# Kernel tuning notes

Measured on AMD Instinct MI355X. Metric: run time of the kernel, lower is better.

Reference implementation:

```python
import jax, jax.numpy as jnp
import numpy as np

D_MODEL = 768
D_FF = 3072
N_HEADS = 12
D_QUART = D_MODEL // 4  # 192
EPS = 1e-5


def layer_norm(x, g, b):
    mu = jnp.mean(x, axis=-1, keepdims=True)
    var = jnp.mean((x - mu) ** 2, axis=-1, keepdims=True)
    return (x - mu) * jax.lax.rsqrt(var + EPS) * g + b


def setup_inputs() -> dict:
    key = jax.random.key(0)
    ks = jax.random.split(key, 24)
    d, dff, dq = D_MODEL, D_FF, D_QUART
    s = lambda k, shape, fan: jax.random.normal(k, shape, jnp.float32) * (1.0 / np.sqrt(fan))
    return {
        "x": jax.random.normal(ks[0], (8, 1024, d), jnp.float32),
        # distance_proj: Linear(1, d//4) -> weight [dq], bias [dq]
        "dp_w": s(ks[1], (dq,), 1), "dp_b": jnp.zeros((dq,), jnp.float32),
        # spatial_encoding: Linear(d,d) GELU Linear(d,d)
        "se_w1": s(ks[2], (d, d), d), "se_b1": jnp.zeros((d,), jnp.float32),
        "se_w2": s(ks[3], (d, d), d), "se_b2": jnp.zeros((d,), jnp.float32),
        # attention projections (stored [in, out])
        "wq": s(ks[4], (d, d), d), "bq": jnp.zeros((d,), jnp.float32),
        "wk": s(ks[5], (d, d), d), "bk": jnp.zeros((d,), jnp.float32),
        "wv": s(ks[6], (d, d), d), "bv": jnp.zeros((d,), jnp.float32),
        "wo": s(ks[7], (d, d), d), "bo": jnp.zeros((d,), jnp.float32),
        # geometric_net FFN
        "gw1": s(ks[8], (d, dff), d), "gb1": jnp.zeros((dff,), jnp.float32),
        "gw2": s(ks[9], (dff, d), dff), "gb2": jnp.zeros((d,), jnp.float32),
        # layer norms
        "n1_g": jnp.ones((d,), jnp.float32), "n1_b": jnp.zeros((d,), jnp.float32),
        "n2_g": jnp.ones((d,), jnp.float32), "n2_b": jnp.zeros((d,), jnp.float32),
    }


def _forward(x, dp_w, dp_b, se_w1, se_b1, se_w2, se_b2,
             wq, bq, wk, bk, wv, bv, wo, bo,
             gw1, gb1, gw2, gb2, n1_g, n1_b, n2_g, n2_b):
    B, N, d = x.shape
    # --- compute_spatial_features ---
    # ||x_i - x_j|| via Gram trick (avoids [B,N,N,d] intermediate)
    sq = jnp.sum(x * x, axis=-1)                      # [B,N]
    gram = jnp.einsum('bnd,bmd->bnm', x, x)           # [B,N,N]
    d2 = jnp.maximum(sq[:, :, None] + sq[:, None, :] - 2.0 * gram, 0.0)
    dist = jnp.sqrt(d2)                               # [B,N,N]
    # Linear(1, d/4) then mean over j commutes: project the mean distance
    mean_d = jnp.mean(dist, axis=2)                   # [B,N]
    spat = mean_d[..., None] * dp_w + dp_b            # [B,N,d/4]
    spat = jnp.pad(spat, ((0, 0), (0, 0), (0, d - D_QUART)))  # [B,N,d]
    # spatial_encoding MLP (exact GELU, matching torch nn.GELU default)
    h = jax.nn.gelu(spat @ se_w1 + se_b1, approximate=False)
    x = x + (h @ se_w2 + se_b2)
    # --- attention block ---
    res = x
    xn = layer_norm(x, n1_g, n1_b)
    H, dh = N_HEADS, d // N_HEADS
    q = (xn @ wq + bq).reshape(B, N, H, dh)
    k = (xn @ wk + bk).reshape(B, N, H, dh)
    v = (xn @ wv + bv).reshape(B, N, H, dh)
    scores = jnp.einsum('bqhd,bkhd->bhqk', q, k) / np.sqrt(dh)
    attn = jax.nn.softmax(scores, axis=-1)
    o = jnp.einsum('bhqk,bkhd->bqhd', attn, v).reshape(B, N, d)
    x = res + (o @ wo + bo)
    # --- FFN block ---
    res = x
    xn = layer_norm(x, n2_g, n2_b)
    h = jax.nn.gelu(xn @ gw1 + gb1, approximate=False)
    x = res + (h @ gw2 + gb2)
    return x


def reference(x, dp_w, dp_b, se_w1, se_b1, se_w2, se_b2,
              wq, bq, wk, bk, wv, bv, wo, bo,
              gw1, gb1, gw2, gb2, n1_g, n1_b, n2_g, n2_b):
    return _forward(x, dp_w, dp_b, se_w1, se_b1, se_w2, se_b2,
                    wq, bq, wk, bk, wv, bv, wo, bo,
                    gw1, gb1, gw2, gb2, n1_g, n1_b, n2_g, n2_b)
```

## Files before the change

kernel.cpp:

```cpp
#include <hip/hip_runtime.h>
#include <hip/hip_bf16.h>

typedef unsigned short ushort;
typedef __attribute__((ext_vector_type(8))) __bf16 bf16x8;
typedef __attribute__((ext_vector_type(4))) float f32x4;
typedef __attribute__((ext_vector_type(8))) ushort ushort8;

__device__ inline ushort f2bf(float f) {
    union { float f; unsigned u; } a{f};
    unsigned r = a.u + 0x7FFFu + ((a.u >> 16) & 1u);
    return (ushort)(r >> 16);
}
__device__ inline float gelu_f(float x) {
    return 0.5f * x * (1.f + erff(x * 0.70710678118654752f));
}

__global__ void transpose_to_bf16(const float* __restrict__ Wm, ushort* __restrict__ Wt, int K, int N) {
    __shared__ float tile[32][33];
    int k0 = blockIdx.x * 32, n0 = blockIdx.y * 32;
    int tx = threadIdx.x, ty = threadIdx.y;
    #pragma unroll
    for (int r = ty; r < 32; r += 8) tile[r][tx] = Wm[(size_t)(k0 + r) * N + n0 + tx];
    __syncthreads();
    #pragma unroll
    for (int r = ty; r < 32; r += 8) Wt[(size_t)(n0 + r) * K + k0 + tx] = f2bf(tile[tx][r]);
}

__global__ void rowstat(const float* __restrict__ x, ushort* __restrict__ xb, float* __restrict__ sq) {
    int row = blockIdx.x;
    const float* xr = x + (size_t)row * 768;
    ushort* xbr = xb + (size_t)row * 768;
    int t = threadIdx.x;
    float s = 0.f;
    #pragma unroll
    for (int i = 0; i < 3; ++i) {
        float vv = xr[t + i * 256];
        xbr[t + i * 256] = f2bf(vv);
        s += vv * vv;
    }
    #pragma unroll
    for (int off = 1; off < 64; off <<= 1) s += __shfl_xor(s, off);
    __shared__ float wsum[4];
    if ((t & 63) == 0) wsum[t >> 6] = s;
    __syncthreads();
    if (t == 0) sq[row] = wsum[0] + wsum[1] + wsum[2] + wsum[3];
}

__global__ void precomp_ac(const float* __restrict__ dp_w, const float* __restrict__ dp_b,
                           const float* __restrict__ se_w1, const float* __restrict__ se_b1,
                           float* __restrict__ Avec, float* __restrict__ Cvec) {
    int o = blockIdx.x * 256 + threadIdx.x;
    float a = 0.f, c = 0.f;
    for (int i = 0; i < 192; ++i) {
        float w = se_w1[(size_t)i * 768 + o];
        a += dp_w[i] * w;
        c += dp_b[i] * w;
    }
    Avec[o] = a;
    Cvec[o] = c + se_b1[o];
}

__global__ void hgen(const float* __restrict__ mean_acc, const float* __restrict__ Avec,
                     const float* __restrict__ Cvec, ushort* __restrict__ h) {
    int row = blockIdx.x;
    float md = mean_acc[row] * (1.f / 1024.f);
    int t = threadIdx.x;
    #pragma unroll
    for (int i = 0; i < 3; ++i) {
        int o = t + i * 256;
        h[(size_t)row * 768 + o] = f2bf(gelu_f(md * Avec[o] + Cvec[o]));
    }
}

__global__ void lnorm(const float* __restrict__ xin, const float* __restrict__ g,
                      const float* __restrict__ b, ushort* __restrict__ xn) {
    int row = blockIdx.x;
    const float* xr = xin + (size_t)row * 768;
    int t = threadIdx.x;
    float v[3];
    float s = 0.f, s2 = 0.f;
    #pragma unroll
    for (int i = 0; i < 3; ++i) {
        v[i] = xr[t + i * 256];
        s += v[i];
        s2 += v[i] * v[i];
    }
    #pragma unroll
    for (int off = 1; off < 64; off <<= 1) { s += __shfl_xor(s, off); s2 += __shfl_xor(s2, off); }
    __shared__ float a0[4], a1[4];
    if ((t & 63) == 0) { a0[t >> 6] = s; a1[t >> 6] = s2; }
    __syncthreads();
    s = a0[0] + a0[1] + a0[2] + a0[3];
    s2 = a1[0] + a1[1] + a1[2] + a1[3];
    float mu = s * (1.f / 768.f);
    float var = s2 * (1.f / 768.f) - mu * mu;
    float rs = rsqrtf(var + 1e-5f);
    #pragma unroll
    for (int i = 0; i < 3; ++i) {
        int o = t + i * 256;
        xn[(size_t)row * 768 + o] = f2bf((v[i] - mu) * rs * g[o] + b[o]);
    }
}

#define BM 128
#define BK 32

enum { EPI_BF16 = 0, EPI_GELU = 1, EPI_RES = 2, EPI_GRAM = 3, EPI_QKV = 4 };

template <int EPI, int BNT>
__launch_bounds__(256, BNT == 64 ? 4 : 2)
__global__ void gemm_bt(const ushort* __restrict__ A, const ushort* __restrict__ Bt,
                        int M, int N, int K,
                        const float* __restrict__ bias,
                        const float* res, float* outf,
                        ushort* __restrict__ outh,
                        const float* __restrict__ sq, float* __restrict__ mean_acc) {
    __shared__ __align__(16) ushort As[2][BM * BK];
    __shared__ __align__(16) ushort Bs[2][BNT * BK];

    unsigned gx = gridDim.x, gy = gridDim.y;
    unsigned flat = blockIdx.x + gx * (blockIdx.y + gy * blockIdx.z);
    unsigned total = gx * gy * gridDim.z;
    unsigned chunk = total >> 3;
    flat = (flat & 7) * chunk + (flat >> 3);
    unsigned bx = flat % gx;
    unsigned rem = flat / gx;
    unsigned by = rem % gy;
    unsigned bz = rem / gy;

    int m0 = bx * BM;
    int n0 = by * BNT;
    if (EPI == EPI_GRAM) {
        A += (size_t)bz * 1024 * 768;
        Bt = A;
        sq += bz * 1024;
        mean_acc += bz * 1024;
    }
    int t = threadIdx.x, w = t >> 6, l = t & 63;
    int lg = l >> 4, li = l & 15;
    constexpr int MI = (BNT == 128) ? 4 : 2;
    int wm = (BNT == 128) ? (w >> 1) * 64 : w * 32;
    int wn = (BNT == 128) ? (w & 1) * 64 : 0;

    int srow = l >> 2, scol = (l & 3) * 8;
    const ushort* agp0 = A + (size_t)(m0 + (2 * w) * 16 + srow) * K + scol;
    const ushort* agp1 = A + (size_t)(m0 + (2 * w + 1) * 16 + srow) * K + scol;
    const ushort* bgp0;
    const ushort* bgp1 = nullptr;
    ushort* la0 = &As[0][(2 * w) * 16 * BK];
    ushort* lb0;
    if (BNT == 128) {
        bgp0 = Bt + (size_t)(n0 + (2 * w) * 16 + srow) * K + scol;
        bgp1 = Bt + (size_t)(n0 + (2 * w + 1) * 16 + srow) * K + scol;
        lb0 = &Bs[0][(2 * w) * 16 * BK];
    } else {
        bgp0 = Bt + (size_t)(n0 + w * 16 + srow) * K + scol;
        lb0 = &Bs[0][w * 16 * BK];
    }

    f32x4 acc[MI][4] = {};

    auto stage = [&](int buf, int kt) {
        size_t ko = (size_t)kt * BK;
        ushort* la = la0 + buf * (BM * BK);
        ushort* lb = lb0 + buf * (BNT * BK);
        __builtin_amdgcn_global_load_lds((const __attribute__((address_space(1))) void*)(agp0 + ko),
                                         (__attribute__((address_space(3))) void*)la, 16, 0, 0);
        __builtin_amdgcn_global_load_lds((const __attribute__((address_space(1))) void*)(agp1 + ko),
                                         (__attribute__((address_space(3))) void*)(la + 16 * BK), 16, 0, 0);
        __builtin_amdgcn_global_load_lds((const __attribute__((address_space(1))) void*)(bgp0 + ko),
                                         (__attribute__((address_space(3))) void*)lb, 16, 0, 0);
        if (BNT == 128)
            __builtin_amdgcn_global_load_lds((const __attribute__((address_space(1))) void*)(bgp1 + ko),
                                             (__attribute__((address_space(3))) void*)(lb + 16 * BK), 16, 0, 0);
    };

    int nk = K / BK;
    stage(0, 0);
    __syncthreads();
    int buf = 0;
    for (int kt = 0; kt < nk; ++kt) {
        if (kt + 1 < nk) stage(buf ^ 1, kt + 1);
        bf16x8 af[MI], bfr[4];
        #pragma unroll
        for (int i = 0; i < MI; ++i)
            af[i] = *reinterpret_cast<const bf16x8*>(&As[buf][(wm + i * 16 + li) * BK + lg * 8]);
        #pragma unroll
        for (int i = 0; i < 4; ++i)
            bfr[i] = *reinterpret_cast<const bf16x8*>(&Bs[buf][(wn + i * 16 + li) * BK + lg * 8]);
        #pragma unroll
        for (int mi = 0; mi < MI; ++mi)
            #pragma unroll
            for (int ni = 0; ni < 4; ++ni)
                acc[mi][ni] = __builtin_amdgcn_mfma_f32_16x16x32_bf16(af[mi], bfr[ni], acc[mi][ni], 0, 0, 0);
        __syncthreads();
        buf ^= 1;
    }

    #pragma unroll
    for (int mi = 0; mi < MI; ++mi) {
        #pragma unroll
        for (int r = 0; r < 4; ++r) {
            int row = m0 + wm + mi * 16 + lg * 4 + r;
            if (EPI == EPI_GRAM) {
                float si = sq[row];
                float s = 0.f;
                #pragma unroll
                for (int ni = 0; ni < 4; ++ni) {
                    int col = n0 + wn + ni * 16 + li;
                    float d2 = si + sq[col] - 2.f * acc[mi][ni][r];
                    s += sqrtf(fmaxf(d2, 0.f));
                }
                s += __shfl_xor(s, 1); s += __shfl_xor(s, 2);
                s += __shfl_xor(s, 4); s += __shfl_xor(s, 8);
                if (li == 0) atomicAdd(&mean_acc[row], s);
            } else {
                #pragma unroll
                for (int ni = 0; ni < 4; ++ni) {
                    int col = n0 + wn + ni * 16 + li;
                    float v = acc[mi][ni][r] + bias[col];
                    if (EPI == EPI_BF16) outh[(size_t)row * N + col] = f2bf(v);
                    if (EPI == EPI_GELU) outh[(size_t)row * N + col] = f2bf(gelu_f(v));
                    if (EPI == EPI_RES) outf[(size_t)row * N + col] = res[(size_t)row * N + col] + v;
                    if (EPI == EPI_QKV) {
                        int which = col / 768;
                        int c2 = col - which * 768;
                        outh[(size_t)which * (8192 * 768) + (size_t)row * 768 + c2] = f2bf(v);
                    }
                }
            }
        }
    }
}

template <int EPI>
__launch_bounds__(512, 2)
__global__ void gemm8(const ushort* __restrict__ A, const ushort* __restrict__ Bt,
                      int M, int N, int K,
                      const float* __restrict__ bias,
                      const float* res, float* outf, ushort* __restrict__ outh) {
    __shared__ __align__(16) ushort As[3][2][128 * 64];
    __shared__ __align__(16) ushort Bs[3][2][64 * 64];

    unsigned gx = gridDim.x;
    unsigned orig = blockIdx.x + gx * blockIdx.y;
    unsigned xcd = orig & 7;
    unsigned q = orig >> 3;
    unsigned mpg = gx >> 3;
    unsigned mloc = q % mpg;
    unsigned n = q / mpg;
    int m0 = (xcd * mpg + mloc) * 256;
    int n0 = n * 128;

    int t = threadIdx.x, w = t >> 6, l = t & 63;
    int lg = l >> 4, li = l & 15;
    int wr = w >> 1, wc = w & 1;
    int ha = wr >> 1;
    int ra = (wr & 1) * 64;

    f32x4 acc[4][4] = {};

    auto stage = [&](int buf, int kt) {
        int k0 = kt * 64;
        #pragma unroll
        for (int h = 0; h < 2; ++h) {
            #pragma unroll
            for (int jj = 0; jj < 2; ++jj) {
                int d = (2 * w + jj) * 1024 + l * 16;
                int dp = d ^ (((d >> 7) & 7) << 4);
                const ushort* src = A + (size_t)(m0 + h * 128 + (dp >> 7)) * K + k0 + ((dp & 127) >> 1);
                __builtin_amdgcn_global_load_lds(
                    (const __attribute__((address_space(1))) void*)src,
                    (__attribute__((address_space(3))) void*)&As[buf][h][(2 * w + jj) * 512], 16, 0, 0);
            }
            {
                int d = w * 1024 + l * 16;
                int dp = d ^ (((d >> 7) & 7) << 4);
                const ushort* src = Bt + (size_t)(n0 + h * 64 + (dp >> 7)) * K + k0 + ((dp & 127) >> 1);
                __builtin_amdgcn_global_load_lds(
                    (const __attribute__((address_space(1))) void*)src,
                    (__attribute__((address_space(3))) void*)&Bs[buf][h][w * 512], 16, 0, 0);
            }
        }
    };

    int nk = K / 64;
    stage(0, 0);
    stage(1, 1);
    stage(2, 2);
    for (int kt = 0; kt < nk; ++kt) {
        int buf = kt % 3;
        if (kt + 2 < nk)      asm volatile("s_waitcnt vmcnt(12)" ::: "memory");
        else if (kt + 1 < nk) asm volatile("s_waitcnt vmcnt(6)" ::: "memory");
        else                  asm volatile("s_waitcnt vmcnt(0)" ::: "memory");
        asm volatile("s_barrier" ::: "memory");
        __builtin_amdgcn_sched_barrier(0);
        #pragma unroll
        for (int kk = 0; kk < 2; ++kk) {
            bf16x8 af[4], bf[4];
            #pragma unroll
            for (int mi = 0; mi < 4; ++mi) {
                int e = (ra + mi * 16 + li) * 128 + kk * 64 + lg * 16;
                int ep = e ^ (((e >> 7) & 7) << 4);
                af[mi] = *reinterpret_cast<const bf16x8*>(&As[buf][ha][ep >> 1]);
            }
            #pragma unroll
            for (int ni = 0; ni < 4; ++ni) {
                int e = (ni * 16 + li) * 128 + kk * 64 + lg * 16;
                int ep = e ^ (((e >> 7) & 7) << 4);
                bf[ni] = *reinterpret_cast<const bf16x8*>(&Bs[buf][wc][ep >> 1]);
            }
            __builtin_amdgcn_s_setprio(1);
            #pragma unroll
            for (int mi = 0; mi < 4; ++mi)
                #pragma unroll
                for (int ni = 0; ni < 4; ++ni)
                    acc[mi][ni] = __builtin_amdgcn_mfma_f32_16x16x32_bf16(af[mi], bf[ni], acc[mi][ni], 0, 0, 0);
            __builtin_amdgcn_s_setprio(0);
        }
        asm volatile("s_barrier" ::: "memory");
        __builtin_amdgcn_sched_barrier(0);
        if (kt + 3 < nk) stage(buf, kt + 3);
    }

    #pragma unroll
    for (int mi = 0; mi < 4; ++mi) {
        #pragma unroll
        for (int r = 0; r < 4; ++r) {
            int row = m0 + wr * 64 + mi * 16 + lg * 4 + r;
            #pragma unroll
            for (int ni = 0; ni < 4; ++ni) {
                int col = n0 + wc * 64 + ni * 16 + li;
                float v = acc[mi][ni][r] + bias[col];
                if (EPI == EPI_GELU) outh[(size_t)row * N + col] = f2bf(gelu_f(v));
                if (EPI == EPI_RES)  outf[(size_t)row * N + col] = res[(size_t)row * N + col] + v;
                if (EPI == EPI_QKV) {
                    int which = col / 768;
                    int c2 = col - which * 768;
                    outh[(size_t)which * (8192 * 768) + (size_t)row * 768 + c2] = f2bf(v);
                }
            }
        }
    }
}

__launch_bounds__(256, 3)
__global__ void flash_attn(const ushort* __restrict__ q, const ushort* __restrict__ k,
                           const ushort* __restrict__ v, ushort* __restrict__ o) {
    int flat = blockIdx.x + 8 * (blockIdx.y + 12 * blockIdx.z);
    flat = (flat & 7) * 96 + (flat >> 3);
    int qt = flat & 7;
    int rem = flat >> 3;
    int h = rem % 12;
    int b = rem / 12;

    int t = threadIdx.x, w = t >> 6, l = t & 63;
    int lg = l >> 4, li = l & 15;

    __shared__ __align__(16) ushort Vt[2][64][72];
    __shared__ __align__(16) ushort P[4][32][72];

    const size_t hoff = (size_t)h * 64;
    const size_t bbase = (size_t)b * 1024 * 768;

    bf16x8 qf[2][2];
    #pragma unroll
    for (int f = 0; f < 2; ++f) {
        int qrow = qt * 128 + w * 32 + f * 16 + li;
        const ushort* qp = &q[bbase + (size_t)qrow * 768 + hoff];
        qf[f][0] = *reinterpret_cast<const bf16x8*>(qp + lg * 8);
        qf[f][1] = *reinterpret_cast<const bf16x8*>(qp + 32 + lg * 8);
    }

    float m_[2][4], ell[2][4];
    f32x4 oacc[2][4];
    #pragma unroll
    for (int f = 0; f < 2; ++f)
        #pragma unroll
        for (int r = 0; r < 4; ++r) { m_[f][r] = -1e30f; ell[f][r] = 0.f; }
    #pragma unroll
    for (int f = 0; f < 2; ++f)
        #pragma unroll
        for (int n = 0; n < 4; ++n) oacc[f][n] = f32x4{0.f, 0.f, 0.f, 0.f};

    int vrow = t & 63;
    int vc = t >> 6;
    const ushort* vbase = &v[bbase + hoff];

    ushort8 vv0 = *reinterpret_cast<const ushort8*>(&vbase[(size_t)vrow * 768 + vc * 8]);
    ushort8 vv1 = *reinterpret_cast<const ushort8*>(&vbase[(size_t)vrow * 768 + (vc + 4) * 8]);

    for (int jt = 0; jt < 16; ++jt) {
        int j0 = jt * 64, buf = jt & 1;
        #pragma unroll
        for (int i = 0; i < 8; ++i) Vt[buf][vc * 8 + i][vrow] = vv0[i];
        #pragma unroll
        for (int i = 0; i < 8; ++i) Vt[buf][(vc + 4) * 8 + i][vrow] = vv1[i];
        if (jt < 15) {
            vv0 = *reinterpret_cast<const ushort8*>(&vbase[(size_t)(j0 + 64 + vrow) * 768 + vc * 8]);
            vv1 = *reinterpret_cast<const ushort8*>(&vbase[(size_t)(j0 + 64 + vrow) * 768 + (vc + 4) * 8]);
        }
        bf16x8 kf0[4], kf1[4];
        #pragma unroll
        for (int jj = 0; jj < 4; ++jj) {
            const ushort* kp = &k[bbase + (size_t)(j0 + jj * 16 + li) * 768 + hoff];
            kf0[jj] = *reinterpret_cast<const bf16x8*>(kp + lg * 8);
            kf1[jj] = *reinterpret_cast<const bf16x8*>(kp + 32 + lg * 8);
        }
        f32x4 s[2][4];
        #pragma unroll
        for (int jj = 0; jj < 4; ++jj)
            #pragma unroll
            for (int f = 0; f < 2; ++f) {
                f32x4 a = {0.f, 0.f, 0.f, 0.f};
                a = __builtin_amdgcn_mfma_f32_16x16x32_bf16(qf[f][0], kf0[jj], a, 0, 0, 0);
                a = __builtin_amdgcn_mfma_f32_16x16x32_bf16(qf[f][1], kf1[jj], a, 0, 0, 0);
                s[f][jj] = a * 0.125f;
            }
        #pragma unroll
        for (int f = 0; f < 2; ++f) {
            float mt[4];
            #pragma unroll
            for (int r = 0; r < 4; ++r)
                mt[r] = fmaxf(fmaxf(s[f][0][r], s[f][1][r]), fmaxf(s[f][2][r], s[f][3][r]));
            #pragma unroll
            for (int r = 0; r < 4; ++r) {
                mt[r] = fmaxf(mt[r], __shfl_xor(mt[r], 1));
                mt[r] = fmaxf(mt[r], __shfl_xor(mt[r], 2));
                mt[r] = fmaxf(mt[r], __shfl_xor(mt[r], 4));
                mt[r] = fmaxf(mt[r], __shfl_xor(mt[r], 8));
            }
            float al[4], ps[4];
            #pragma unroll
            for (int r = 0; r < 4; ++r) {
                float mn = fmaxf(m_[f][r], mt[r]);
                al[r] = __expf(m_[f][r] - mn);
                m_[f][r] = mn;
                float p0 = __expf(s[f][0][r] - mn);
                float p1 = __expf(s[f][1][r] - mn);
                float p2 = __expf(s[f][2][r] - mn);
                float p3 = __expf(s[f][3][r] - mn);
                s[f][0][r] = p0; s[f][1][r] = p1; s[f][2][r] = p2; s[f][3][r] = p3;
                ps[r] = (p0 + p1) + (p2 + p3);
            }
            #pragma unroll
            for (int r = 0; r < 4; ++r) {
                ps[r] += __shfl_xor(ps[r], 1); ps[r] += __shfl_xor(ps[r], 2);
                ps[r] += __shfl_xor(ps[r], 4); ps[r] += __shfl_xor(ps[r], 8);
                ell[f][r] = ell[f][r] * al[r] + ps[r];
            }
            #pragma unroll
            for (int n = 0; n < 4; ++n)
                #pragma unroll
                for (int r = 0; r < 4; ++r) oacc[f][n][r] *= al[r];
            #pragma unroll
            for (int jj = 0; jj < 4; ++jj)
                #pragma unroll
                for (int r = 0; r < 4; ++r)
                    P[w][f * 16 + lg * 4 + r][jj * 16 + li] = f2bf(s[f][jj][r]);
        }
        __syncthreads();
        bf16x8 pf[2][2];
        #pragma unroll
        for (int f = 0; f < 2; ++f) {
            pf[f][0] = *reinterpret_cast<const bf16x8*>(&P[w][f * 16 + li][lg * 8]);
            pf[f][1] = *reinterpret_cast<const bf16x8*>(&P[w][f * 16 + li][32 + lg * 8]);
        }
        #pragma unroll
        for (int n = 0; n < 4; ++n) {
            bf16x8 vf0 = *reinterpret_cast<const bf16x8*>(&Vt[buf][n * 16 + li][lg * 8]);
            bf16x8 vf1 = *reinterpret_cast<const bf16x8*>(&Vt[buf][n * 16 + li][32 + lg * 8]);
            #pragma unroll
            for (int f = 0; f < 2; ++f) {
                oacc[f][n] = __builtin_amdgcn_mfma_f32_16x16x32_bf16(pf[f][0], vf0, oacc[f][n], 0, 0, 0);
                oacc[f][n] = __builtin_amdgcn_mfma_f32_16x16x32_bf16(pf[f][1], vf1, oacc[f][n], 0, 0, 0);
            }
        }
    }
    #pragma unroll
    for (int f = 0; f < 2; ++f)
        #pragma unroll
        for (int n = 0; n < 4; ++n)
            #pragma unroll
            for (int r = 0; r < 4; ++r) {
                int row = qt * 128 + w * 32 + f * 16 + lg * 4 + r;
                o[bbase + (size_t)row * 768 + hoff + n * 16 + li] = f2bf(oacc[f][n][r] / ell[f][r]);
            }
}

extern "C" void kernel_launch(void* const* d_in, const int* in_sizes, int n_in,
                              void* d_out, int out_size, void* d_ws, size_t ws_size,
                              hipStream_t stream) {
    const float* x = (const float*)d_in[0];
    const float* dp_w = (const float*)d_in[1];
    const float* dp_b = (const float*)d_in[2];
    const float* se_w1 = (const float*)d_in[3];
    const float* se_b1 = (const float*)d_in[4];
    const float* se_w2 = (const float*)d_in[5];
    const float* se_b2 = (const float*)d_in[6];
    const float* wq = (const float*)d_in[7];  const float* bq = (const float*)d_in[8];
    const float* wk = (const float*)d_in[9];  const float* bk = (const float*)d_in[10];
    const float* wv = (const float*)d_in[11]; const float* bv = (const float*)d_in[12];
    const float* wo = (const float*)d_in[13]; const float* bo = (const float*)d_in[14];
    const float* gw1 = (const float*)d_in[15]; const float* gb1 = (const float*)d_in[16];
    const float* gw2 = (const float*)d_in[17]; const float* gb2 = (const float*)d_in[18];
    const float* n1g = (const float*)d_in[19]; const float* n1b = (const float*)d_in[20];
    const float* n2g = (const float*)d_in[21]; const float* n2b = (const float*)d_in[22];
    float* out = (float*)d_out;

    constexpr size_t SZ_ACT = (size_t)8192 * 768 * 2;
    char* W = (char*)d_ws;
    ushort* xb = (ushort*)(W);
    ushort* q_ = (ushort*)(W + SZ_ACT);
    ushort* k_ = (ushort*)(W + 2 * SZ_ACT);
    ushort* v_ = (ushort*)(W + 3 * SZ_ACT);
    ushort* o_ = (ushort*)(W + 4 * SZ_ACT);
    ushort* hsp = q_;
    ushort* hff = q_;
    ushort* wqt = (ushort*)(W + 5 * SZ_ACT);
    ushort* wkt = wqt + (size_t)768 * 768;
    ushort* wvt = wkt + (size_t)768 * 768;
    ushort* wot = wvt + (size_t)768 * 768;
    ushort* sw2t = wot + (size_t)768 * 768;
    ushort* g1t = sw2t + (size_t)768 * 768;
    ushort* g2t = g1t + (size_t)768 * 3072;
    float* sqv = (float*)(g2t + (size_t)3072 * 768);
    float* meanv = sqv + 8192;
    float* Avec = meanv + 8192;
    float* Cvec = Avec + 768;
    float* bqkv = Cvec + 768;

    dim3 tb(32, 8);
    transpose_to_bf16<<<dim3(24, 24), tb, 0, stream>>>(se_w2, sw2t, 768, 768);
    transpose_to_bf16<<<dim3(24, 24), tb, 0, stream>>>(wq, wqt, 768, 768);
    transpose_to_bf16<<<dim3(24, 24), tb, 0, stream>>>(wk, wkt, 768, 768);
    transpose_to_bf16<<<dim3(24, 24), tb, 0, stream>>>(wv, wvt, 768, 768);
    transpose_to_bf16<<<dim3(24, 24), tb, 0, stream>>>(wo, wot, 768, 768);
    transpose_to_bf16<<<dim3(24, 96), tb, 0, stream>>>(gw1, g1t, 768, 3072);
    transpose_to_bf16<<<dim3(96, 24), tb, 0, stream>>>(gw2, g2t, 3072, 768);
    hipMemcpyAsync(bqkv, bq, 768 * sizeof(float), hipMemcpyDeviceToDevice, stream);
    hipMemcpyAsync(bqkv + 768, bk, 768 * sizeof(float), hipMemcpyDeviceToDevice, stream);
    hipMemcpyAsync(bqkv + 1536, bv, 768 * sizeof(float), hipMemcpyDeviceToDevice, stream);

    rowstat<<<8192, 256, 0, stream>>>(x, xb, sqv);
    precomp_ac<<<3, 256, 0, stream>>>(dp_w, dp_b, se_w1, se_b1, Avec, Cvec);
    hipMemsetAsync(meanv, 0, 8192 * sizeof(float), stream);

    gemm_bt<EPI_GRAM, 128><<<dim3(8, 8, 8), 256, 0, stream>>>(xb, xb, 1024, 1024, 768,
                                                              nullptr, nullptr, nullptr, nullptr, sqv, meanv);
    hgen<<<8192, 256, 0, stream>>>(meanv, Avec, Cvec, hsp);
    gemm8<EPI_RES><<<dim3(32, 6), 512, 0, stream>>>(hsp, sw2t, 8192, 768, 768,
                                                    se_b2, x, out, nullptr);
    lnorm<<<8192, 256, 0, stream>>>(out, n1g, n1b, xb);
    gemm8<EPI_QKV><<<dim3(32, 18), 512, 0, stream>>>(xb, wqt, 8192, 2304, 768,
                                                     bqkv, nullptr, nullptr, q_);
    flash_attn<<<dim3(8, 12, 8), 256, 0, stream>>>(q_, k_, v_, o_);
    gemm8<EPI_RES><<<dim3(32, 6), 512, 0, stream>>>(o_, wot, 8192, 768, 768,
                                                    bo, out, out, nullptr);
    lnorm<<<8192, 256, 0, stream>>>(out, n2g, n2b, xb);
    gemm8<EPI_GELU><<<dim3(32, 24), 512, 0, stream>>>(xb, g1t, 8192, 3072, 768,
                                                      gb1, nullptr, nullptr, hff);
    gemm8<EPI_RES><<<dim3(32, 6), 512, 0, stream>>>(hff, g2t, 8192, 768, 3072,
                                                    gb2, out, out, nullptr);
}
```

Measured before the change: 475.9 us.

## Split flash attention over two KV halves and merge partials

The flash attention kernel now splits each query tile's key/value range into two halves, doubling the grid from 768 to 1536 blocks for better CU occupancy, and raises launch bounds to 4 blocks per CU. Each half writes unnormalized bf16 partial outputs plus per-row max and sum, and a new merge kernel combines them with log-sum-exp rescaling. This adds an extra kernel launch, partial-output traffic through the xb buffer, and some rounding error from storing unnormalized partials in bf16.

```diff
diff --git a/kernel.cpp b/kernel.cpp
--- a/kernel.cpp
+++ b/kernel.cpp
@@ -10,6 +10,10 @@
     union { float f; unsigned u; } a{f};
     unsigned r = a.u + 0x7FFFu + ((a.u >> 16) & 1u);
     return (ushort)(r >> 16);
+}
+__device__ inline float bf2f(ushort u) {
+    union { unsigned u; float f; } a{(unsigned)u << 16};
+    return a.f;
 }
 __device__ inline float gelu_f(float x) {
     return 0.5f * x * (1.f + erff(x * 0.70710678118654752f));
@@ -344,13 +348,16 @@
     }
 }
 
-__launch_bounds__(256, 3)
+__launch_bounds__(256, 4)
 __global__ void flash_attn(const ushort* __restrict__ q, const ushort* __restrict__ k,
-                           const ushort* __restrict__ v, ushort* __restrict__ o) {
-    int flat = blockIdx.x + 8 * (blockIdx.y + 12 * blockIdx.z);
-    flat = (flat & 7) * 96 + (flat >> 3);
+                           const ushort* __restrict__ v,
+                           ushort* __restrict__ po0, ushort* __restrict__ po1,
+                           float* __restrict__ pm, float* __restrict__ pe) {
+    int flat = blockIdx.x + 16 * (blockIdx.y + 12 * blockIdx.z);
+    flat = (flat & 7) * 192 + (flat >> 3);
     int qt = flat & 7;
-    int rem = flat >> 3;
+    int split = (flat >> 3) & 1;
+    int rem = flat >> 4;
     int h = rem % 12;
     int b = rem / 12;
 
@@ -387,16 +394,17 @@
     int vc = t >> 6;
     const ushort* vbase = &v[bbase + hoff];
 
-    ushort8 vv0 = *reinterpret_cast<const ushort8*>(&vbase[(size_t)vrow * 768 + vc * 8]);
-    ushort8 vv1 = *reinterpret_cast<const ushort8*>(&vbase[(size_t)vrow * 768 + (vc + 4) * 8]);
-
-    for (int jt = 0; jt < 16; ++jt) {
+    const int jts = split * 8;
+    ushort8 vv0 = *reinterpret_cast<const ushort8*>(&vbase[(size_t)(jts * 64 + vrow) * 768 + vc * 8]);
+    ushort8 vv1 = *reinterpret_cast<const ushort8*>(&vbase[(size_t)(jts * 64 + vrow) * 768 + (vc + 4) * 8]);
+
+    for (int jt = jts; jt < jts + 8; ++jt) {
         int j0 = jt * 64, buf = jt & 1;
         #pragma unroll
         for (int i = 0; i < 8; ++i) Vt[buf][vc * 8 + i][vrow] = vv0[i];
         #pragma unroll
         for (int i = 0; i < 8; ++i) Vt[buf][(vc + 4) * 8 + i][vrow] = vv1[i];
-        if (jt < 15) {
+        if (jt < jts + 7) {
             vv0 = *reinterpret_cast<const ushort8*>(&vbase[(size_t)(j0 + 64 + vrow) * 768 + vc * 8]);
             vv1 = *reinterpret_cast<const ushort8*>(&vbase[(size_t)(j0 + 64 + vrow) * 768 + (vc + 4) * 8]);
         }
@@ -477,6 +485,7 @@
             }
         }
     }
+    ushort* po = split ? po1 : po0;
     #pragma unroll
     for (int f = 0; f < 2; ++f)
         #pragma unroll
@@ -484,8 +493,47 @@
             #pragma unroll
             for (int r = 0; r < 4; ++r) {
                 int row = qt * 128 + w * 32 + f * 16 + lg * 4 + r;
-                o[bbase + (size_t)row * 768 + hoff + n * 16 + li] = f2bf(oacc[f][n][r] / ell[f][r]);
-            }
+                po[bbase + (size_t)row * 768 + hoff + n * 16 + li] = f2bf(oacc[f][n][r]);
+            }
+    if (li == 0) {
+        #pragma unroll
+        for (int f = 0; f < 2; ++f)
+            #pragma unroll
+            for (int r = 0; r < 4; ++r) {
+                int rowl = qt * 128 + w * 32 + f * 16 + lg * 4 + r;
+                size_t si = (((size_t)split * 8 + b) * 12 + h) * 1024 + rowl;
+                pm[si] = m_[f][r];
+                pe[si] = ell[f][r];
+            }
+    }
+}
+
+__launch_bounds__(128)
+__global__ void merge_attn(const ushort* __restrict__ po0, const ushort* __restrict__ po1,
+                           const float* __restrict__ pm, const float* __restrict__ pe,
+                           ushort* __restrict__ o) {
+    int row = blockIdx.x;
+    int b = row >> 10, n = row & 1023;
+    int t = threadIdx.x;
+    if (t >= 96) return;
+    int c = t * 8;
+    int h = c >> 6;
+    size_t si0 = ((size_t)b * 12 + h) * 1024 + n;
+    size_t si1 = ((size_t)(8 + b) * 12 + h) * 1024 + n;
+    float m0 = pm[si0], m1 = pm[si1];
+    float e0 = pe[si0], e1 = pe[si1];
+    float m = fmaxf(m0, m1);
+    float a0 = __expf(m0 - m), a1 = __expf(m1 - m);
+    float inv = 1.f / (a0 * e0 + a1 * e1);
+    a0 *= inv; a1 *= inv;
+    size_t idx = (size_t)row * 768 + c;
+    ushort8 u0 = *reinterpret_cast<const ushort8*>(&po0[idx]);
+    ushort8 u1 = *reinterpret_cast<const ushort8*>(&po1[idx]);
+    ushort8 rr;
+    #pragma unroll
+    for (int i = 0; i < 8; ++i)
+        rr[i] = f2bf(a0 * bf2f(u0[i]) + a1 * bf2f(u1[i]));
+    *reinterpret_cast<ushort8*>(&o[idx]) = rr;
 }
 
 extern "C" void kernel_launch(void* const* d_in, const int* in_sizes, int n_in,
@@ -529,6 +577,8 @@
     float* Avec = meanv + 8192;
     float* Cvec = Avec + 768;
     float* bqkv = Cvec + 768;
+    float* pm = bqkv + 2304;
+    float* pe = pm + 2 * 8 * 12 * 1024;
 
     dim3 tb(32, 8);
     transpose_to_bf16<<<dim3(24, 24), tb, 0, stream>>>(se_w2, sw2t, 768, 768);
@@ -554,7 +604,8 @@
     lnorm<<<8192, 256, 0, stream>>>(out, n1g, n1b, xb);
     gemm8<EPI_QKV><<<dim3(32, 18), 512, 0, stream>>>(xb, wqt, 8192, 2304, 768,
                                                      bqkv, nullptr, nullptr, q_);
-    flash_attn<<<dim3(8, 12, 8), 256, 0, stream>>>(q_, k_, v_, o_);
+    flash_attn<<<dim3(16, 12, 8), 256, 0, stream>>>(q_, k_, v_, o_, xb, pm, pe);
+    merge_attn<<<8192, 128, 0, stream>>>(o_, xb, pm, pe, o_);
     gemm8<EPI_RES><<<dim3(32, 6), 512, 0, stream>>>(o_, wot, 8192, 768, 768,
                                                     bo, out, out, nullptr);
     lnorm<<<8192, 256, 0, stream>>>(out, n2g, n2b, xb);
```

After: 492.5 us. 1.04x slower.

## Use lazy max rescaling and MFMA row-sum in flash attention softmax

Applied to the files above, without the earlier changes.

Changes the online softmax in the attention kernel in two ways. The running max and output rescale are updated only when some row's new tile max exceeds the stored max by more than a threshold of 8, otherwise exponentials use the stale max. The per-row sum of probabilities is now computed by an extra MFMA against a ones vector instead of shuffle reductions. This removes shuffles and per-tile rescaling work, at the cost of extra MFMAs, a wave-wide branch, and a possible loss of precision because probabilities up to e^8 are stored in bf16.

```diff
diff --git a/kernel.cpp b/kernel.cpp
--- a/kernel.cpp
+++ b/kernel.cpp
@@ -372,16 +372,21 @@
         qf[f][1] = *reinterpret_cast<const bf16x8*>(qp + 32 + lg * 8);
     }
 
-    float m_[2][4], ell[2][4];
+    bf16x8 onesf;
+    #pragma unroll
+    for (int i = 0; i < 8; ++i) onesf[i] = (__bf16)1.0f;
+
+    float m_[2][4];
     f32x4 oacc[2][4];
-    #pragma unroll
-    for (int f = 0; f < 2; ++f)
-        #pragma unroll
-        for (int r = 0; r < 4; ++r) { m_[f][r] = -1e30f; ell[f][r] = 0.f; }
-    #pragma unroll
-    for (int f = 0; f < 2; ++f)
+    f32x4 oell[2];
+    #pragma unroll
+    for (int f = 0; f < 2; ++f) {
+        #pragma unroll
+        for (int r = 0; r < 4; ++r) m_[f][r] = -1e30f;
+        oell[f] = f32x4{0.f, 0.f, 0.f, 0.f};
         #pragma unroll
         for (int n = 0; n < 4; ++n) oacc[f][n] = f32x4{0.f, 0.f, 0.f, 0.f};
+    }
 
     int vrow = t & 63;
     int vc = t >> 6;
@@ -430,34 +435,24 @@
                 mt[r] = fmaxf(mt[r], __shfl_xor(mt[r], 4));
                 mt[r] = fmaxf(mt[r], __shfl_xor(mt[r], 8));
             }
-            float al[4], ps[4];
-            #pragma unroll
-            for (int r = 0; r < 4; ++r) {
-                float mn = fmaxf(m_[f][r], mt[r]);
-                al[r] = __expf(m_[f][r] - mn);
-                m_[f][r] = mn;
-                float p0 = __expf(s[f][0][r] - mn);
-                float p1 = __expf(s[f][1][r] - mn);
-                float p2 = __expf(s[f][2][r] - mn);
-                float p3 = __expf(s[f][3][r] - mn);
-                s[f][0][r] = p0; s[f][1][r] = p1; s[f][2][r] = p2; s[f][3][r] = p3;
-                ps[r] = (p0 + p1) + (p2 + p3);
-            }
-            #pragma unroll
-            for (int r = 0; r < 4; ++r) {
-                ps[r] += __shfl_xor(ps[r], 1); ps[r] += __shfl_xor(ps[r], 2);
-                ps[r] += __shfl_xor(ps[r], 4); ps[r] += __shfl_xor(ps[r], 8);
-                ell[f][r] = ell[f][r] * al[r] + ps[r];
-            }
-            #pragma unroll
-            for (int n = 0; n < 4; ++n)
+            bool need = (mt[0] > m_[f][0] + 8.f) | (mt[1] > m_[f][1] + 8.f) |
+                        (mt[2] > m_[f][2] + 8.f) | (mt[3] > m_[f][3] + 8.f);
+            if (__any(need)) {
                 #pragma unroll
-                for (int r = 0; r < 4; ++r) oacc[f][n][r] *= al[r];
+                for (int r = 0; r < 4; ++r) {
+                    float mn = fmaxf(m_[f][r], mt[r]);
+                    float al = __expf(m_[f][r] - mn);
+                    m_[f][r] = mn;
+                    #pragma unroll
+                    for (int n = 0; n < 4; ++n) oacc[f][n][r] *= al;
+                    oell[f][r] *= al;
+                }
+            }
             #pragma unroll
             for (int jj = 0; jj < 4; ++jj)
                 #pragma unroll
                 for (int r = 0; r < 4; ++r)
-                    P[w][f * 16 + lg * 4 + r][jj * 16 + li] = f2bf(s[f][jj][r]);
+                    P[w][f * 16 + lg * 4 + r][jj * 16 + li] = f2bf(__expf(s[f][jj][r] - m_[f][r]));
         }
         __syncthreads();
         bf16x8 pf[2][2];
@@ -467,6 +462,11 @@
             pf[f][1] = *reinterpret_cast<const bf16x8*>(&P[w][f * 16 + li][32 + lg * 8]);
         }
         #pragma unroll
+        for (int f = 0; f < 2; ++f) {
+            oell[f] = __builtin_amdgcn_mfma_f32_16x16x32_bf16(pf[f][0], onesf, oell[f], 0, 0, 0);
+            oell[f] = __builtin_amdgcn_mfma_f32_16x16x32_bf16(pf[f][1], onesf, oell[f], 0, 0, 0);
+        }
+        #pragma unroll
         for (int n = 0; n < 4; ++n) {
             bf16x8 vf0 = *reinterpret_cast<const bf16x8*>(&Vt[buf][n * 16 + li][lg * 8]);
             bf16x8 vf1 = *reinterpret_cast<const bf16x8*>(&Vt[buf][n * 16 + li][32 + lg * 8]);
@@ -484,7 +484,7 @@
             #pragma unroll
             for (int r = 0; r < 4; ++r) {
                 int row = qt * 128 + w * 32 + f * 16 + lg * 4 + r;
-                o[bbase + (size_t)row * 768 + hoff + n * 16 + li] = f2bf(oacc[f][n][r] / ell[f][r]);
+                o[bbase + (size_t)row * 768 + hoff + n * 16 + li] = f2bf(oacc[f][n][r] / oell[f][r]);
             }
 }
 
```

Measured after the change: 458.9 us. 1.04x faster.
